# Kernel tuning notes

Measured on AMD Instinct MI355X. Metric: run time of the kernel, lower is better.

The kernel has to match this reference:

```python
import jax, jax.numpy as jnp
import numpy as np

S, B, D, H, A = 256, 1024, 64, 128, 8  # seq_len, buffer, state_size, hidden, action_size


def _init(key, shape, fan_in):
    bound = 1.0 / np.sqrt(fan_in)
    return jax.random.uniform(key, shape, jnp.float32, -bound, bound)


def setup_inputs() -> dict:
    key = jax.random.key(0)
    ks = jax.random.split(key, 24)
    inp = {"state": jax.random.normal(ks[0], (S, B, D), jnp.float32)}
    # actor / critic MLPs (Linear(D,H) + ReLU + Linear(H,H) + ReLU)
    inp["aw1"] = _init(ks[1], (H, D), D); inp["ab1"] = _init(ks[2], (H,), D)
    inp["aw2"] = _init(ks[3], (H, H), H); inp["ab2"] = _init(ks[4], (H,), H)
    inp["cw1"] = _init(ks[5], (H, D), D); inp["cb1"] = _init(ks[6], (H,), D)
    inp["cw2"] = _init(ks[7], (H, H), H); inp["cb2"] = _init(ks[8], (H,), H)
    # LSTMs (PyTorch layout: W_ih [4H,H], W_hh [4H,H], gate order i,f,g,o)
    inp["a_wih"] = _init(ks[9], (4 * H, H), H); inp["a_whh"] = _init(ks[10], (4 * H, H), H)
    inp["a_bih"] = _init(ks[11], (4 * H,), H); inp["a_bhh"] = _init(ks[12], (4 * H,), H)
    inp["c_wih"] = _init(ks[13], (4 * H, H), H); inp["c_whh"] = _init(ks[14], (4 * H, H), H)
    inp["c_bih"] = _init(ks[15], (4 * H,), H); inp["c_bhh"] = _init(ks[16], (4 * H,), H)
    # heads
    inp["mw"] = _init(ks[17], (A, H), H); inp["mb"] = _init(ks[18], (A,), H)
    inp["lw"] = _init(ks[19], (A, H), H); inp["lb"] = _init(ks[20], (A,), H)
    inp["vw"] = _init(ks[21], (1, H), H); inp["vb"] = _init(ks[22], (1,), H)
    return inp


def _mlp(x, w1, b1, w2, b2):
    h = jax.nn.relu(jnp.einsum('sbd,hd->sbh', x, w1) + b1)
    return jax.nn.relu(jnp.einsum('sbh,gh->sbg', h, w2) + b2)


def _lstm_zero_state(x, w_ih, b_ih, b_hh):
    # Each timestep runs with fresh zero (h, c): the recurrent term vanishes,
    # so the whole sequence is one batched GEMM + gating (W_hh unused).
    gates = jnp.einsum('sbh,gh->sbg', x, w_ih) + b_ih + b_hh  # [S,B,4H]
    i, f, g, o = jnp.split(gates, 4, axis=-1)
    c = jax.nn.sigmoid(i) * jnp.tanh(g)  # f * c_prev = 0
    return jax.nn.sigmoid(o) * jnp.tanh(c)


def reference(state, aw1, ab1, aw2, ab2, cw1, cb1, cw2, cb2,
              a_wih, a_whh, a_bih, a_bhh, c_wih, c_whh, c_bih, c_bhh,
              mw, mb, lw, lb, vw, vb):
    actor_h = _lstm_zero_state(_mlp(state, aw1, ab1, aw2, ab2), a_wih, a_bih, a_bhh)
    critic_h = _lstm_zero_state(_mlp(state, cw1, cb1, cw2, cb2), c_wih, c_bih, c_bhh)
    mean = jnp.einsum('sbh,ah->sba', actor_h, mw) + mb
    std = jnp.exp(jnp.einsum('sbh,ah->sba', actor_h, lw) + lb)
    value = jnp.einsum('sbh,vh->sbv', critic_h, vw) + vb
    return (mean, std, value)
```

## Files before the change

kernel.cpp:

```cpp
#include <hip/hip_runtime.h>


#define NROWS (256 * 1024)
#define HID 128
#define ACTD 8

#define W1_OFF 0
#define W2_OFF 16384
#define WI_OFF 49152
#define WG_OFF 81920
#define WO_OFF 114688
#define PSTR 147456
#define HEAD_OFF (2 * PSTR)
#define GB_OFF (HEAD_OFF + 8192)

#define NEG_L (-1.4426950408889634f)
#define TWO_L (2.8853900817779268f)

typedef __attribute__((ext_vector_type(8))) short s16x8;
typedef __attribute__((ext_vector_type(4))) float fx4;
typedef __attribute__((ext_vector_type(2))) unsigned int u32x2;
typedef __attribute__((ext_vector_type(4))) unsigned int u32x4;

__device__ __forceinline__ unsigned int cvtpk(float lo, float hi) {
  unsigned int r;
  asm("v_cvt_pk_bf16_f32 %0, %1, %2" : "=v"(r) : "v"(lo), "v"(hi));
  return r;
}
__device__ __forceinline__ float ex2(float x) {
  return __builtin_amdgcn_exp2f(x);
}
__device__ __forceinline__ float frcp(float x) {
  return __builtin_amdgcn_rcpf(x);
}

__device__ __forceinline__ s16x8 frag_ld(const unsigned short* base, int row,
                                         int kbyte, int rowsh) {
  int byte = (row << rowsh) + (kbyte ^ ((row & 7) << 4));
  return *(const s16x8*)((const char*)base + byte);
}

struct wpair {
  s16x8 w0, w1;
};
template <int KC>
__device__ __forceinline__ wpair wload(const char* __restrict__ wimg, int wv,
                                       int kc, int woff) {
  wpair p;
  p.w0 = *(const s16x8*)(wimg + (((wv * 2 + 0) * KC + kc) << 10) + woff);
  p.w1 = *(const s16x8*)(wimg + (((wv * 2 + 1) * KC + kc) << 10) + woff);
  return p;
}

template <int ASH>
__device__ __forceinline__ void gemm_kc(const wpair& p,
                                        const unsigned short* at, int kbyte,
                                        int l15, fx4 acc[4][2]) {
#pragma unroll
  for (int jt = 0; jt < 4; ++jt) {
    s16x8 a = frag_ld(at, jt * 16 + l15, kbyte, ASH);
    acc[jt][0] = __builtin_amdgcn_mfma_f32_16x16x32_bf16(p.w0, a, acc[jt][0], 0, 0, 0);
    acc[jt][1] = __builtin_amdgcn_mfma_f32_16x16x32_bf16(p.w1, a, acc[jt][1], 0, 0, 0);
  }
}

__device__ __forceinline__ void zacc(fx4 acc[4][2]) {
#pragma unroll
  for (int j = 0; j < 4; ++j)
#pragma unroll
    for (int i = 0; i < 2; ++i) acc[j][i] = fx4{0.f, 0.f, 0.f, 0.f};
}
__device__ __forceinline__ void bacc(fx4 acc[4][2], const float* __restrict__ b,
                                     int fb, int g4) {
#pragma unroll
  for (int it = 0; it < 2; ++it) {
    fx4 bv = *(const fx4*)(b + fb + it * 16 + g4);
#pragma unroll
    for (int jt = 0; jt < 4; ++jt) acc[jt][it] = bv;
  }
}

__device__ __forceinline__ void epi_relu(fx4 acc[4][2], unsigned short* obuf,
                                         int fb, int lane) {
  const int g4 = (lane >> 4) << 2;
  const int l15 = lane & 15;
  char* ob = (char*)obuf;
#pragma unroll
  for (int it = 0; it < 2; ++it) {
    int n0 = fb + it * 16 + g4;
#pragma unroll
    for (int jt = 0; jt < 4; ++jt) {
      fx4 v = acc[jt][it];
#pragma unroll
      for (int r = 0; r < 4; ++r) v[r] = fmaxf(v[r], 0.0f);
      u32x2 u;
      u[0] = cvtpk(v[0], v[1]);
      u[1] = cvtpk(v[2], v[3]);
      int m = jt * 16 + l15;
      *(u32x2*)(ob + (m << 8) + ((n0 * 2) ^ ((m & 7) << 4))) = u;
    }
  }
}

__global__ void prep_weights(const float* __restrict__ aw1,
                             const float* __restrict__ aw2,
                             const float* __restrict__ awih,
                             const float* __restrict__ cw1,
                             const float* __restrict__ cw2,
                             const float* __restrict__ cwih,
                             const float* __restrict__ mw,
                             const float* __restrict__ lw,
                             const float* __restrict__ vw,
                             const float* __restrict__ abih,
                             const float* __restrict__ abhh,
                             const float* __restrict__ cbih,
                             const float* __restrict__ cbhh,
                             char* __restrict__ ws) {
  int y = blockIdx.y;
  int idx = blockIdx.x * 256 + threadIdx.x;
  if (y >= 12) {
    if (idx < 384) {
      float* dst = (float*)(ws + GB_OFF + (size_t)(y - 12) * 1536);
      const float* b0 = (y == 12) ? abih : cbih;
      const float* b1 = (y == 12) ? abhh : cbhh;
      int sect = idx >> 7, f = idx & 127;
      int srow = (sect == 0) ? f : (sect == 1) ? 256 + f : 384 + f;
      float scale = (sect == 1) ? TWO_L : NEG_L;
      dst[idx] = scale * (b0[srow] + b1[srow]);
    }
    return;
  }
  if (y >= 10) {
    if (idx >= 256) return;
    int row = idx >> 4, c16 = idx & 15, kc = c16 >> 2, ks = c16 & 3;
    fx4 v0 = {0.f, 0.f, 0.f, 0.f}, v1 = v0;
    if (y == 10) {
      const float* src = (row < 8) ? (mw + (size_t)row * HID + c16 * 8)
                                   : (lw + (size_t)(row - 8) * HID + c16 * 8);
      v0 = ((const fx4*)src)[0];
      v1 = ((const fx4*)src)[1];
    } else if (row == 0) {
      const float* src = vw + c16 * 8;
      v0 = ((const fx4*)src)[0];
      v1 = ((const fx4*)src)[1];
    }
    u32x4 u;
    u[0] = cvtpk(v0[0], v0[1]);
    u[1] = cvtpk(v0[2], v0[3]);
    u[2] = cvtpk(v1[0], v1[1]);
    u[3] = cvtpk(v1[2], v1[3]);
    int dst = ((kc * 4 + ks) * 16 + row) * 16;
    *(u32x4*)(ws + HEAD_OFF + (size_t)(y - 10) * 4096 + dst) = u;
    return;
  }
  const float* src;
  int nch, ksh, KC, off;
  switch (y) {
    case 0:  src = aw1;              nch = 1024; ksh = 3; KC = 2; off = W1_OFF;        break;
    case 1:  src = aw2;              nch = 2048; ksh = 4; KC = 4; off = W2_OFF;        break;
    case 2:  src = awih;             nch = 2048; ksh = 4; KC = 4; off = WI_OFF;        break;
    case 3:  src = awih + 256 * HID; nch = 2048; ksh = 4; KC = 4; off = WG_OFF;        break;
    case 4:  src = awih + 384 * HID; nch = 2048; ksh = 4; KC = 4; off = WO_OFF;        break;
    case 5:  src = cw1;              nch = 1024; ksh = 3; KC = 2; off = PSTR + W1_OFF; break;
    case 6:  src = cw2;              nch = 2048; ksh = 4; KC = 4; off = PSTR + W2_OFF; break;
    case 7:  src = cwih;             nch = 2048; ksh = 4; KC = 4; off = PSTR + WI_OFF; break;
    case 8:  src = cwih + 256 * HID; nch = 2048; ksh = 4; KC = 4; off = PSTR + WG_OFF; break;
    default: src = cwih + 384 * HID; nch = 2048; ksh = 4; KC = 4; off = PSTR + WO_OFF; break;
  }
  if (idx >= nch) return;
  int row = idx >> ksh;
  int c16 = idx & ((1 << ksh) - 1);
  int b2 = row >> 4, r = row & 15, kc = c16 >> 2, ks = c16 & 3;
  const fx4* gp = (const fx4*)(src + (size_t)idx * 8);
  fx4 v0 = gp[0], v1 = gp[1];
  u32x4 u;
  u[0] = cvtpk(v0[0], v0[1]);
  u[1] = cvtpk(v0[2], v0[3]);
  u[2] = cvtpk(v1[0], v1[1]);
  u[3] = cvtpk(v1[2], v1[3]);
  int dst = (((b2 * KC + kc) * 4 + ks) * 16 + r) * 16;
  *(u32x4*)(ws + off + dst) = u;
}

__global__ __launch_bounds__(256, 3) void fused_ac(
    const float* __restrict__ state, const float* __restrict__ ab1,
    const float* __restrict__ ab2, const float* __restrict__ cb1,
    const float* __restrict__ cb2, const float* __restrict__ mb,
    const float* __restrict__ lb, const float* __restrict__ vb,
    const char* __restrict__ ws, float* __restrict__ outp) {
  __shared__ __align__(16) unsigned short abuf[8192];
  __shared__ __align__(16) unsigned short hbuf[8192];

  const int tid = threadIdx.x;
  const int lane = tid & 63;
  const int wv = tid >> 6;
  const int l15 = lane & 15;
  const int g4 = (lane >> 4) << 2;
  const int kb0 = (lane >> 4) << 4;
  const int woff = ((lane >> 4) << 8) + (l15 << 4);
  const int fb = wv << 5;
  const int path = blockIdx.x >> 12;
  const int rbase = (blockIdx.x & 4095) << 6;

  const char* wsp = ws + (size_t)path * PSTR;
  const float* b1 = path ? cb1 : ab1;
  const float* b2 = path ? cb2 : ab2;
  const float* gb = (const float*)(ws + GB_OFF + (size_t)path * 1536);
  const char* himg = ws + HEAD_OFF + (size_t)path * 4096;

  float* meanp = outp;
  float* stdp = outp + (size_t)NROWS * ACTD;
  float* valp = outp + (size_t)NROWS * ACTD * 2;

  wpair w1a = wload<2>(wsp + W1_OFF, wv, 0, woff);
  wpair w1b = wload<2>(wsp + W1_OFF, wv, 1, woff);

  {
    const float* xg = state + (size_t)rbase * 64;
    char* ab = (char*)abuf;
#pragma unroll
    for (int i = 0; i < 2; ++i) {
      int idx = tid + i * 256;
      int r = idx >> 3, c = idx & 7;
      const fx4* gp = (const fx4*)(xg + idx * 8);
      fx4 v0 = gp[0], v1 = gp[1];
      u32x4 u;
      u[0] = cvtpk(v0[0], v0[1]);
      u[1] = cvtpk(v0[2], v0[3]);
      u[2] = cvtpk(v1[0], v1[1]);
      u[3] = cvtpk(v1[2], v1[3]);
      *(u32x4*)(ab + r * 128 + ((c << 4) ^ ((r & 7) << 4))) = u;
    }
  }
  __syncthreads();

  fx4 acc[4][2];
  bacc(acc, b1, fb, g4);
  gemm_kc<7>(w1a, abuf, 0 + kb0, l15, acc);
  gemm_kc<7>(w1b, abuf, 64 + kb0, l15, acc);
  wpair w2a = wload<4>(wsp + W2_OFF, wv, 0, woff);
  wpair w2b = wload<4>(wsp + W2_OFF, wv, 1, woff);
  epi_relu(acc, hbuf, fb, lane);
  __syncthreads();

  bacc(acc, b2, fb, g4);
  gemm_kc<8>(w2a, hbuf, 0 + kb0, l15, acc);
  gemm_kc<8>(w2b, hbuf, 64 + kb0, l15, acc);
  {
    wpair p = wload<4>(wsp + W2_OFF, wv, 2, woff);
    gemm_kc<8>(p, hbuf, 128 + kb0, l15, acc);
  }
  {
    wpair p = wload<4>(wsp + W2_OFF, wv, 3, woff);
    gemm_kc<8>(p, hbuf, 192 + kb0, l15, acc);
  }
  wpair wia = wload<4>(wsp + WI_OFF, wv, 0, woff);
  wpair wib = wload<4>(wsp + WI_OFF, wv, 1, woff);
  epi_relu(acc, abuf, fb, lane);
  __syncthreads();

  fx4 carry[4][2];
  zacc(acc);
  gemm_kc<8>(wia, abuf, 0 + kb0, l15, acc);
  gemm_kc<8>(wib, abuf, 64 + kb0, l15, acc);
  {
    wpair p = wload<4>(wsp + WI_OFF, wv, 2, woff);
    gemm_kc<8>(p, abuf, 128 + kb0, l15, acc);
  }
  {
    wpair p = wload<4>(wsp + WI_OFF, wv, 3, woff);
    gemm_kc<8>(p, abuf, 192 + kb0, l15, acc);
  }
#pragma unroll
  for (int it = 0; it < 2; ++it) {
    fx4 pv = *(const fx4*)(gb + fb + it * 16 + g4);
#pragma unroll
    for (int jt = 0; jt < 4; ++jt)
#pragma unroll
      for (int r = 0; r < 4; ++r)
        carry[jt][it][r] = ex2(fmaf(acc[jt][it][r], NEG_L, pv[r]));
  }

  zacc(acc);
#pragma unroll
  for (int kc = 0; kc < 4; ++kc) {
    wpair p = wload<4>(wsp + WG_OFF, wv, kc, woff);
    gemm_kc<8>(p, abuf, kc * 64 + kb0, l15, acc);
  }
#pragma unroll
  for (int it = 0; it < 2; ++it) {
    fx4 pv = *(const fx4*)(gb + 128 + fb + it * 16 + g4);
#pragma unroll
    for (int jt = 0; jt < 4; ++jt)
#pragma unroll
      for (int r = 0; r < 4; ++r) {
        float Eg = ex2(fmaf(acc[jt][it][r], TWO_L, pv[r]));
        float c = (Eg - 1.0f) * frcp((Eg + 1.0f) * (carry[jt][it][r] + 1.0f));
        carry[jt][it][r] = ex2(c * TWO_L);
      }
  }

  zacc(acc);
#pragma unroll
  for (int kc = 0; kc < 4; ++kc) {
    wpair p = wload<4>(wsp + WO_OFF, wv, kc, woff);
    gemm_kc<8>(p, abuf, kc * 64 + kb0, l15, acc);
  }
  s16x8 hw0 = *(const s16x8*)(himg + (0 << 10) + woff);
  s16x8 hw1 = *(const s16x8*)(himg + (1 << 10) + woff);
  s16x8 hw2 = *(const s16x8*)(himg + (2 << 10) + woff);
  s16x8 hw3 = *(const s16x8*)(himg + (3 << 10) + woff);
  {
    char* ob = (char*)hbuf;
#pragma unroll
    for (int it = 0; it < 2; ++it) {
      fx4 pv = *(const fx4*)(gb + 256 + fb + it * 16 + g4);
      int n0 = fb + it * 16 + g4;
#pragma unroll
      for (int jt = 0; jt < 4; ++jt) {
        fx4 h;
#pragma unroll
        for (int r = 0; r < 4; ++r) {
          float Eo = ex2(fmaf(acc[jt][it][r], NEG_L, pv[r]));
          float Ec = carry[jt][it][r];
          h[r] = (Ec - 1.0f) * frcp((Ec + 1.0f) * (Eo + 1.0f));
        }
        u32x2 u;
        u[0] = cvtpk(h[0], h[1]);
        u[1] = cvtpk(h[2], h[3]);
        int m = jt * 16 + l15;
        *(u32x2*)(ob + (m << 8) + ((n0 * 2) ^ ((m & 7) << 4))) = u;
      }
    }
  }
  __syncthreads();

  fx4 ha = fx4{0.f, 0.f, 0.f, 0.f};
  ha = __builtin_amdgcn_mfma_f32_16x16x32_bf16(
      hw0, frag_ld(hbuf, (wv << 4) + l15, 0 + kb0, 8), ha, 0, 0, 0);
  ha = __builtin_amdgcn_mfma_f32_16x16x32_bf16(
      hw1, frag_ld(hbuf, (wv << 4) + l15, 64 + kb0, 8), ha, 0, 0, 0);
  ha = __builtin_amdgcn_mfma_f32_16x16x32_bf16(
      hw2, frag_ld(hbuf, (wv << 4) + l15, 128 + kb0, 8), ha, 0, 0, 0);
  ha = __builtin_amdgcn_mfma_f32_16x16x32_bf16(
      hw3, frag_ld(hbuf, (wv << 4) + l15, 192 + kb0, 8), ha, 0, 0, 0);

  int m = rbase + (wv << 4) + l15;
  if (path == 0) {
    if (g4 < 8) {
      fx4 v = ha + *(const fx4*)(mb + g4);
      *(fx4*)(meanp + (size_t)m * ACTD + g4) = v;
    } else {
      fx4 v;
#pragma unroll
      for (int r = 0; r < 4; ++r) v[r] = __expf(ha[r] + lb[g4 - 8 + r]);
      *(fx4*)(stdp + (size_t)m * ACTD + (g4 - 8)) = v;
    }
  } else if (g4 == 0) {
    valp[m] = ha[0] + vb[0];
  }
}

extern "C" void kernel_launch(void* const* d_in, const int* in_sizes, int n_in,
                              void* d_out, int out_size, void* d_ws,
                              size_t ws_size, hipStream_t stream) {
  (void)in_sizes; (void)n_in; (void)ws_size; (void)out_size;
  const float* state = (const float*)d_in[0];
  const float* aw1 = (const float*)d_in[1];
  const float* ab1 = (const float*)d_in[2];
  const float* aw2 = (const float*)d_in[3];
  const float* ab2 = (const float*)d_in[4];
  const float* cw1 = (const float*)d_in[5];
  const float* cb1 = (const float*)d_in[6];
  const float* cw2 = (const float*)d_in[7];
  const float* cb2 = (const float*)d_in[8];
  const float* awih = (const float*)d_in[9];
  const float* abih = (const float*)d_in[11];
  const float* abhh = (const float*)d_in[12];
  const float* cwih = (const float*)d_in[13];
  const float* cbih = (const float*)d_in[15];
  const float* cbhh = (const float*)d_in[16];
  const float* mw = (const float*)d_in[17];
  const float* mb = (const float*)d_in[18];
  const float* lw = (const float*)d_in[19];
  const float* lb = (const float*)d_in[20];
  const float* vw = (const float*)d_in[21];
  const float* vb = (const float*)d_in[22];
  char* ws = (char*)d_ws;

  prep_weights<<<dim3(8, 14), 256, 0, stream>>>(
      aw1, aw2, awih, cw1, cw2, cwih, mw, lw, vw, abih, abhh, cbih, cbhh, ws);
  fused_ac<<<8192, 256, 0, stream>>>(state, ab1, ab2, cb1, cb2, mb, lb, vb, ws,
                                     (float*)d_out);
}
```

Measured before the change: 120.1 us.

## Split work across 8 waves per block, one 16-column tile each

Doubles the block to 512 threads so each of the 8 waves computes a single 16-wide feature slice instead of two. This halves per-wave accumulator and weight registers and raises the number of resident waves. The state load now uses one element per thread, and only the first four waves run the head GEMM. In exchange, each wave reloads the shared activation fragments for half as much MFMA work, so LDS traffic per MFMA doubles, and the head phase leaves half the waves idle.

```diff
diff --git a/kernel.cpp b/kernel.cpp
--- a/kernel.cpp
+++ b/kernel.cpp
@@ -40,65 +40,50 @@
   return *(const s16x8*)((const char*)base + byte);
 }
 
-struct wpair {
-  s16x8 w0, w1;
-};
 template <int KC>
-__device__ __forceinline__ wpair wload(const char* __restrict__ wimg, int wv,
-                                       int kc, int woff) {
-  wpair p;
-  p.w0 = *(const s16x8*)(wimg + (((wv * 2 + 0) * KC + kc) << 10) + woff);
-  p.w1 = *(const s16x8*)(wimg + (((wv * 2 + 1) * KC + kc) << 10) + woff);
-  return p;
+__device__ __forceinline__ s16x8 wload1(const char* __restrict__ wimg, int wv,
+                                        int kc, int woff) {
+  return *(const s16x8*)(wimg + ((wv * KC + kc) << 10) + woff);
 }
 
 template <int ASH>
-__device__ __forceinline__ void gemm_kc(const wpair& p,
+__device__ __forceinline__ void gemm_kc(const s16x8 w,
                                         const unsigned short* at, int kbyte,
-                                        int l15, fx4 acc[4][2]) {
+                                        int l15, fx4 acc[4]) {
 #pragma unroll
   for (int jt = 0; jt < 4; ++jt) {
     s16x8 a = frag_ld(at, jt * 16 + l15, kbyte, ASH);
-    acc[jt][0] = __builtin_amdgcn_mfma_f32_16x16x32_bf16(p.w0, a, acc[jt][0], 0, 0, 0);
-    acc[jt][1] = __builtin_amdgcn_mfma_f32_16x16x32_bf16(p.w1, a, acc[jt][1], 0, 0, 0);
-  }
-}
-
-__device__ __forceinline__ void zacc(fx4 acc[4][2]) {
-#pragma unroll
-  for (int j = 0; j < 4; ++j)
-#pragma unroll
-    for (int i = 0; i < 2; ++i) acc[j][i] = fx4{0.f, 0.f, 0.f, 0.f};
-}
-__device__ __forceinline__ void bacc(fx4 acc[4][2], const float* __restrict__ b,
+    acc[jt] = __builtin_amdgcn_mfma_f32_16x16x32_bf16(w, a, acc[jt], 0, 0, 0);
+  }
+}
+
+__device__ __forceinline__ void zacc(fx4 acc[4]) {
+#pragma unroll
+  for (int j = 0; j < 4; ++j) acc[j] = fx4{0.f, 0.f, 0.f, 0.f};
+}
+__device__ __forceinline__ void bacc(fx4 acc[4], const float* __restrict__ b,
                                      int fb, int g4) {
-#pragma unroll
-  for (int it = 0; it < 2; ++it) {
-    fx4 bv = *(const fx4*)(b + fb + it * 16 + g4);
-#pragma unroll
-    for (int jt = 0; jt < 4; ++jt) acc[jt][it] = bv;
-  }
-}
-
-__device__ __forceinline__ void epi_relu(fx4 acc[4][2], unsigned short* obuf,
+  fx4 bv = *(const fx4*)(b + fb + g4);
+#pragma unroll
+  for (int jt = 0; jt < 4; ++jt) acc[jt] = bv;
+}
+
+__device__ __forceinline__ void epi_relu(fx4 acc[4], unsigned short* obuf,
                                          int fb, int lane) {
   const int g4 = (lane >> 4) << 2;
   const int l15 = lane & 15;
+  const int n0 = fb + g4;
   char* ob = (char*)obuf;
 #pragma unroll
-  for (int it = 0; it < 2; ++it) {
-    int n0 = fb + it * 16 + g4;
-#pragma unroll
-    for (int jt = 0; jt < 4; ++jt) {
-      fx4 v = acc[jt][it];
-#pragma unroll
-      for (int r = 0; r < 4; ++r) v[r] = fmaxf(v[r], 0.0f);
-      u32x2 u;
-      u[0] = cvtpk(v[0], v[1]);
-      u[1] = cvtpk(v[2], v[3]);
-      int m = jt * 16 + l15;
-      *(u32x2*)(ob + (m << 8) + ((n0 * 2) ^ ((m & 7) << 4))) = u;
-    }
+  for (int jt = 0; jt < 4; ++jt) {
+    fx4 v = acc[jt];
+#pragma unroll
+    for (int r = 0; r < 4; ++r) v[r] = fmaxf(v[r], 0.0f);
+    u32x2 u;
+    u[0] = cvtpk(v[0], v[1]);
+    u[1] = cvtpk(v[2], v[3]);
+    int m = jt * 16 + l15;
+    *(u32x2*)(ob + (m << 8) + ((n0 * 2) ^ ((m & 7) << 4))) = u;
   }
 }
 
@@ -182,7 +167,7 @@
   *(u32x4*)(ws + off + dst) = u;
 }
 
-__global__ __launch_bounds__(256, 3) void fused_ac(
+__global__ __launch_bounds__(512, 4) void fused_ac(
     const float* __restrict__ state, const float* __restrict__ ab1,
     const float* __restrict__ ab2, const float* __restrict__ cb1,
     const float* __restrict__ cb2, const float* __restrict__ mb,
@@ -198,7 +183,7 @@
   const int g4 = (lane >> 4) << 2;
   const int kb0 = (lane >> 4) << 4;
   const int woff = ((lane >> 4) << 8) + (l15 << 4);
-  const int fb = wv << 5;
+  const int fb = wv << 4;
   const int path = blockIdx.x >> 12;
   const int rbase = (blockIdx.x & 4095) << 6;
 
@@ -212,152 +197,134 @@
   float* stdp = outp + (size_t)NROWS * ACTD;
   float* valp = outp + (size_t)NROWS * ACTD * 2;
 
-  wpair w1a = wload<2>(wsp + W1_OFF, wv, 0, woff);
-  wpair w1b = wload<2>(wsp + W1_OFF, wv, 1, woff);
+  s16x8 w1a = wload1<2>(wsp + W1_OFF, wv, 0, woff);
+  s16x8 w1b = wload1<2>(wsp + W1_OFF, wv, 1, woff);
 
   {
     const float* xg = state + (size_t)rbase * 64;
     char* ab = (char*)abuf;
-#pragma unroll
-    for (int i = 0; i < 2; ++i) {
-      int idx = tid + i * 256;
-      int r = idx >> 3, c = idx & 7;
-      const fx4* gp = (const fx4*)(xg + idx * 8);
-      fx4 v0 = gp[0], v1 = gp[1];
-      u32x4 u;
-      u[0] = cvtpk(v0[0], v0[1]);
-      u[1] = cvtpk(v0[2], v0[3]);
-      u[2] = cvtpk(v1[0], v1[1]);
-      u[3] = cvtpk(v1[2], v1[3]);
-      *(u32x4*)(ab + r * 128 + ((c << 4) ^ ((r & 7) << 4))) = u;
-    }
+    int r = tid >> 3, c = tid & 7;
+    const fx4* gp = (const fx4*)(xg + tid * 8);
+    fx4 v0 = gp[0], v1 = gp[1];
+    u32x4 u;
+    u[0] = cvtpk(v0[0], v0[1]);
+    u[1] = cvtpk(v0[2], v0[3]);
+    u[2] = cvtpk(v1[0], v1[1]);
+    u[3] = cvtpk(v1[2], v1[3]);
+    *(u32x4*)(ab + r * 128 + ((c << 4) ^ ((r & 7) << 4))) = u;
   }
   __syncthreads();
 
-  fx4 acc[4][2];
+  fx4 acc[4];
   bacc(acc, b1, fb, g4);
   gemm_kc<7>(w1a, abuf, 0 + kb0, l15, acc);
   gemm_kc<7>(w1b, abuf, 64 + kb0, l15, acc);
-  wpair w2a = wload<4>(wsp + W2_OFF, wv, 0, woff);
-  wpair w2b = wload<4>(wsp + W2_OFF, wv, 1, woff);
+  s16x8 w2a = wload1<4>(wsp + W2_OFF, wv, 0, woff);
+  s16x8 w2b = wload1<4>(wsp + W2_OFF, wv, 1, woff);
   epi_relu(acc, hbuf, fb, lane);
   __syncthreads();
 
   bacc(acc, b2, fb, g4);
   gemm_kc<8>(w2a, hbuf, 0 + kb0, l15, acc);
   gemm_kc<8>(w2b, hbuf, 64 + kb0, l15, acc);
-  {
-    wpair p = wload<4>(wsp + W2_OFF, wv, 2, woff);
-    gemm_kc<8>(p, hbuf, 128 + kb0, l15, acc);
-  }
-  {
-    wpair p = wload<4>(wsp + W2_OFF, wv, 3, woff);
-    gemm_kc<8>(p, hbuf, 192 + kb0, l15, acc);
-  }
-  wpair wia = wload<4>(wsp + WI_OFF, wv, 0, woff);
-  wpair wib = wload<4>(wsp + WI_OFF, wv, 1, woff);
+  gemm_kc<8>(wload1<4>(wsp + W2_OFF, wv, 2, woff), hbuf, 128 + kb0, l15, acc);
+  gemm_kc<8>(wload1<4>(wsp + W2_OFF, wv, 3, woff), hbuf, 192 + kb0, l15, acc);
+  s16x8 wia = wload1<4>(wsp + WI_OFF, wv, 0, woff);
+  s16x8 wib = wload1<4>(wsp + WI_OFF, wv, 1, woff);
   epi_relu(acc, abuf, fb, lane);
   __syncthreads();
 
-  fx4 carry[4][2];
+  fx4 carry[4];
   zacc(acc);
   gemm_kc<8>(wia, abuf, 0 + kb0, l15, acc);
   gemm_kc<8>(wib, abuf, 64 + kb0, l15, acc);
+  gemm_kc<8>(wload1<4>(wsp + WI_OFF, wv, 2, woff), abuf, 128 + kb0, l15, acc);
+  gemm_kc<8>(wload1<4>(wsp + WI_OFF, wv, 3, woff), abuf, 192 + kb0, l15, acc);
   {
-    wpair p = wload<4>(wsp + WI_OFF, wv, 2, woff);
-    gemm_kc<8>(p, abuf, 128 + kb0, l15, acc);
-  }
+    fx4 pv = *(const fx4*)(gb + fb + g4);
+#pragma unroll
+    for (int jt = 0; jt < 4; ++jt)
+#pragma unroll
+      for (int r = 0; r < 4; ++r)
+        carry[jt][r] = ex2(fmaf(acc[jt][r], NEG_L, pv[r]));
+  }
+
+  zacc(acc);
+#pragma unroll
+  for (int kc = 0; kc < 4; ++kc)
+    gemm_kc<8>(wload1<4>(wsp + WG_OFF, wv, kc, woff), abuf, kc * 64 + kb0,
+               l15, acc);
   {
-    wpair p = wload<4>(wsp + WI_OFF, wv, 3, woff);
-    gemm_kc<8>(p, abuf, 192 + kb0, l15, acc);
-  }
-#pragma unroll
-  for (int it = 0; it < 2; ++it) {
-    fx4 pv = *(const fx4*)(gb + fb + it * 16 + g4);
+    fx4 pv = *(const fx4*)(gb + 128 + fb + g4);
 #pragma unroll
     for (int jt = 0; jt < 4; ++jt)
 #pragma unroll
-      for (int r = 0; r < 4; ++r)
-        carry[jt][it][r] = ex2(fmaf(acc[jt][it][r], NEG_L, pv[r]));
+      for (int r = 0; r < 4; ++r) {
+        float Eg = ex2(fmaf(acc[jt][r], TWO_L, pv[r]));
+        float c = (Eg - 1.0f) * frcp((Eg + 1.0f) * (carry[jt][r] + 1.0f));
+        carry[jt][r] = ex2(c * TWO_L);
+      }
   }
 
   zacc(acc);
 #pragma unroll
-  for (int kc = 0; kc < 4; ++kc) {
-    wpair p = wload<4>(wsp + WG_OFF, wv, kc, woff);
-    gemm_kc<8>(p, abuf, kc * 64 + kb0, l15, acc);
-  }
-#pragma unroll
-  for (int it = 0; it < 2; ++it) {
-    fx4 pv = *(const fx4*)(gb + 128 + fb + it * 16 + g4);
-#pragma unroll
-    for (int jt = 0; jt < 4; ++jt)
-#pragma unroll
-      for (int r = 0; r < 4; ++r) {
-        float Eg = ex2(fmaf(acc[jt][it][r], TWO_L, pv[r]));
-        float c = (Eg - 1.0f) * frcp((Eg + 1.0f) * (carry[jt][it][r] + 1.0f));
-        carry[jt][it][r] = ex2(c * TWO_L);
-      }
-  }
-
-  zacc(acc);
-#pragma unroll
-  for (int kc = 0; kc < 4; ++kc) {
-    wpair p = wload<4>(wsp + WO_OFF, wv, kc, woff);
-    gemm_kc<8>(p, abuf, kc * 64 + kb0, l15, acc);
-  }
-  s16x8 hw0 = *(const s16x8*)(himg + (0 << 10) + woff);
-  s16x8 hw1 = *(const s16x8*)(himg + (1 << 10) + woff);
-  s16x8 hw2 = *(const s16x8*)(himg + (2 << 10) + woff);
-  s16x8 hw3 = *(const s16x8*)(himg + (3 << 10) + woff);
+  for (int kc = 0; kc < 4; ++kc)
+    gemm_kc<8>(wload1<4>(wsp + WO_OFF, wv, kc, woff), abuf, kc * 64 + kb0,
+               l15, acc);
+  s16x8 hw0, hw1, hw2, hw3;
+  if (wv < 4) {
+    hw0 = *(const s16x8*)(himg + (0 << 10) + woff);
+    hw1 = *(const s16x8*)(himg + (1 << 10) + woff);
+    hw2 = *(const s16x8*)(himg + (2 << 10) + woff);
+    hw3 = *(const s16x8*)(himg + (3 << 10) + woff);
+  }
   {
     char* ob = (char*)hbuf;
-#pragma unroll
-    for (int it = 0; it < 2; ++it) {
-      fx4 pv = *(const fx4*)(gb + 256 + fb + it * 16 + g4);
-      int n0 = fb + it * 16 + g4;
-#pragma unroll
-      for (int jt = 0; jt < 4; ++jt) {
-        fx4 h;
-#pragma unroll
-        for (int r = 0; r < 4; ++r) {
-          float Eo = ex2(fmaf(acc[jt][it][r], NEG_L, pv[r]));
-          float Ec = carry[jt][it][r];
-          h[r] = (Ec - 1.0f) * frcp((Ec + 1.0f) * (Eo + 1.0f));
-        }
-        u32x2 u;
-        u[0] = cvtpk(h[0], h[1]);
-        u[1] = cvtpk(h[2], h[3]);
-        int m = jt * 16 + l15;
-        *(u32x2*)(ob + (m << 8) + ((n0 * 2) ^ ((m & 7) << 4))) = u;
+    fx4 pv = *(const fx4*)(gb + 256 + fb + g4);
+    const int n0 = fb + g4;
+#pragma unroll
+    for (int jt = 0; jt < 4; ++jt) {
+      fx4 h;
+#pragma unroll
+      for (int r = 0; r < 4; ++r) {
+        float Eo = ex2(fmaf(acc[jt][r], NEG_L, pv[r]));
+        float Ec = carry[jt][r];
+        h[r] = (Ec - 1.0f) * frcp((Ec + 1.0f) * (Eo + 1.0f));
       }
+      u32x2 u;
+      u[0] = cvtpk(h[0], h[1]);
+      u[1] = cvtpk(h[2], h[3]);
+      int m = jt * 16 + l15;
+      *(u32x2*)(ob + (m << 8) + ((n0 * 2) ^ ((m & 7) << 4))) = u;
     }
   }
   __syncthreads();
 
-  fx4 ha = fx4{0.f, 0.f, 0.f, 0.f};
-  ha = __builtin_amdgcn_mfma_f32_16x16x32_bf16(
-      hw0, frag_ld(hbuf, (wv << 4) + l15, 0 + kb0, 8), ha, 0, 0, 0);
-  ha = __builtin_amdgcn_mfma_f32_16x16x32_bf16(
-      hw1, frag_ld(hbuf, (wv << 4) + l15, 64 + kb0, 8), ha, 0, 0, 0);
-  ha = __builtin_amdgcn_mfma_f32_16x16x32_bf16(
-      hw2, frag_ld(hbuf, (wv << 4) + l15, 128 + kb0, 8), ha, 0, 0, 0);
-  ha = __builtin_amdgcn_mfma_f32_16x16x32_bf16(
-      hw3, frag_ld(hbuf, (wv << 4) + l15, 192 + kb0, 8), ha, 0, 0, 0);
-
-  int m = rbase + (wv << 4) + l15;
-  if (path == 0) {
-    if (g4 < 8) {
-      fx4 v = ha + *(const fx4*)(mb + g4);
-      *(fx4*)(meanp + (size_t)m * ACTD + g4) = v;
-    } else {
-      fx4 v;
-#pragma unroll
-      for (int r = 0; r < 4; ++r) v[r] = __expf(ha[r] + lb[g4 - 8 + r]);
-      *(fx4*)(stdp + (size_t)m * ACTD + (g4 - 8)) = v;
+  if (wv < 4) {
+    fx4 ha = fx4{0.f, 0.f, 0.f, 0.f};
+    ha = __builtin_amdgcn_mfma_f32_16x16x32_bf16(
+        hw0, frag_ld(hbuf, (wv << 4) + l15, 0 + kb0, 8), ha, 0, 0, 0);
+    ha = __builtin_amdgcn_mfma_f32_16x16x32_bf16(
+        hw1, frag_ld(hbuf, (wv << 4) + l15, 64 + kb0, 8), ha, 0, 0, 0);
+    ha = __builtin_amdgcn_mfma_f32_16x16x32_bf16(
+        hw2, frag_ld(hbuf, (wv << 4) + l15, 128 + kb0, 8), ha, 0, 0, 0);
+    ha = __builtin_amdgcn_mfma_f32_16x16x32_bf16(
+        hw3, frag_ld(hbuf, (wv << 4) + l15, 192 + kb0, 8), ha, 0, 0, 0);
+
+    int m = rbase + (wv << 4) + l15;
+    if (path == 0) {
+      if (g4 < 8) {
+        fx4 v = ha + *(const fx4*)(mb + g4);
+        *(fx4*)(meanp + (size_t)m * ACTD + g4) = v;
+      } else {
+        fx4 v;
+#pragma unroll
+        for (int r = 0; r < 4; ++r) v[r] = __expf(ha[r] + lb[g4 - 8 + r]);
+        *(fx4*)(stdp + (size_t)m * ACTD + (g4 - 8)) = v;
+      }
+    } else if (g4 == 0) {
+      valp[m] = ha[0] + vb[0];
     }
-  } else if (g4 == 0) {
-    valp[m] = ha[0] + vb[0];
   }
 }
 
@@ -390,6 +357,6 @@
 
   prep_weights<<<dim3(8, 14), 256, 0, stream>>>(
       aw1, aw2, awih, cw1, cw2, cwih, mw, lw, vw, abih, abhh, cbih, cbhh, ws);
-  fused_ac<<<8192, 256, 0, stream>>>(state, ab1, ab2, cb1, cb2, mb, lb, vb, ws,
+  fused_ac<<<8192, 512, 0, stream>>>(state, ab1, ab2, cb1, cb2, mb, lb, vb, ws,
                                      (float*)d_out);
 }
```

New measurement: 128.9 us. 1.07x slower.

## Fuse the three LSTM gate GEMMs into one K loop sharing A fragments

Applied to the files above, without the earlier changes.

The i, g and o gate GEMMs are merged into a single K loop. Each activation fragment loaded from LDS now feeds all three gates' MFMAs, instead of being reloaded in three separate passes. The gating math moves into a single epilogue. This cuts LDS fragment reads by a factor of three and gives the scheduler more independent MFMAs, but triples live accumulator registers (24 fx4 accumulators plus weight pairs), which risks lower occupancy or spills.

```diff
diff --git a/kernel.cpp b/kernel.cpp
--- a/kernel.cpp
+++ b/kernel.cpp
@@ -254,75 +254,56 @@
     wpair p = wload<4>(wsp + W2_OFF, wv, 3, woff);
     gemm_kc<8>(p, hbuf, 192 + kb0, l15, acc);
   }
-  wpair wia = wload<4>(wsp + WI_OFF, wv, 0, woff);
-  wpair wib = wload<4>(wsp + WI_OFF, wv, 1, woff);
+  wpair pi0 = wload<4>(wsp + WI_OFF, wv, 0, woff);
+  wpair pg0 = wload<4>(wsp + WG_OFF, wv, 0, woff);
+  wpair po0 = wload<4>(wsp + WO_OFF, wv, 0, woff);
   epi_relu(acc, abuf, fb, lane);
   __syncthreads();
 
-  fx4 carry[4][2];
-  zacc(acc);
-  gemm_kc<8>(wia, abuf, 0 + kb0, l15, acc);
-  gemm_kc<8>(wib, abuf, 64 + kb0, l15, acc);
-  {
-    wpair p = wload<4>(wsp + WI_OFF, wv, 2, woff);
-    gemm_kc<8>(p, abuf, 128 + kb0, l15, acc);
-  }
-  {
-    wpair p = wload<4>(wsp + WI_OFF, wv, 3, woff);
-    gemm_kc<8>(p, abuf, 192 + kb0, l15, acc);
-  }
-#pragma unroll
-  for (int it = 0; it < 2; ++it) {
-    fx4 pv = *(const fx4*)(gb + fb + it * 16 + g4);
-#pragma unroll
-    for (int jt = 0; jt < 4; ++jt)
-#pragma unroll
-      for (int r = 0; r < 4; ++r)
-        carry[jt][it][r] = ex2(fmaf(acc[jt][it][r], NEG_L, pv[r]));
-  }
-
-  zacc(acc);
+  fx4 ai[4][2], ag[4][2], ao[4][2];
+  zacc(ai);
+  zacc(ag);
+  zacc(ao);
 #pragma unroll
   for (int kc = 0; kc < 4; ++kc) {
-    wpair p = wload<4>(wsp + WG_OFF, wv, kc, woff);
-    gemm_kc<8>(p, abuf, kc * 64 + kb0, l15, acc);
-  }
-#pragma unroll
-  for (int it = 0; it < 2; ++it) {
-    fx4 pv = *(const fx4*)(gb + 128 + fb + it * 16 + g4);
-#pragma unroll
-    for (int jt = 0; jt < 4; ++jt)
-#pragma unroll
-      for (int r = 0; r < 4; ++r) {
-        float Eg = ex2(fmaf(acc[jt][it][r], TWO_L, pv[r]));
-        float c = (Eg - 1.0f) * frcp((Eg + 1.0f) * (carry[jt][it][r] + 1.0f));
-        carry[jt][it][r] = ex2(c * TWO_L);
-      }
-  }
-
-  zacc(acc);
-#pragma unroll
-  for (int kc = 0; kc < 4; ++kc) {
-    wpair p = wload<4>(wsp + WO_OFF, wv, kc, woff);
-    gemm_kc<8>(p, abuf, kc * 64 + kb0, l15, acc);
+    wpair pi = (kc == 0) ? pi0 : wload<4>(wsp + WI_OFF, wv, kc, woff);
+    wpair pg = (kc == 0) ? pg0 : wload<4>(wsp + WG_OFF, wv, kc, woff);
+    wpair po = (kc == 0) ? po0 : wload<4>(wsp + WO_OFF, wv, kc, woff);
+    int kbyte = kc * 64 + kb0;
+#pragma unroll
+    for (int jt = 0; jt < 4; ++jt) {
+      s16x8 a = frag_ld(abuf, jt * 16 + l15, kbyte, 8);
+      ai[jt][0] = __builtin_amdgcn_mfma_f32_16x16x32_bf16(pi.w0, a, ai[jt][0], 0, 0, 0);
+      ai[jt][1] = __builtin_amdgcn_mfma_f32_16x16x32_bf16(pi.w1, a, ai[jt][1], 0, 0, 0);
+      ag[jt][0] = __builtin_amdgcn_mfma_f32_16x16x32_bf16(pg.w0, a, ag[jt][0], 0, 0, 0);
+      ag[jt][1] = __builtin_amdgcn_mfma_f32_16x16x32_bf16(pg.w1, a, ag[jt][1], 0, 0, 0);
+      ao[jt][0] = __builtin_amdgcn_mfma_f32_16x16x32_bf16(po.w0, a, ao[jt][0], 0, 0, 0);
+      ao[jt][1] = __builtin_amdgcn_mfma_f32_16x16x32_bf16(po.w1, a, ao[jt][1], 0, 0, 0);
+    }
   }
   s16x8 hw0 = *(const s16x8*)(himg + (0 << 10) + woff);
   s16x8 hw1 = *(const s16x8*)(himg + (1 << 10) + woff);
   s16x8 hw2 = *(const s16x8*)(himg + (2 << 10) + woff);
   s16x8 hw3 = *(const s16x8*)(himg + (3 << 10) + woff);
+
   {
     char* ob = (char*)hbuf;
 #pragma unroll
     for (int it = 0; it < 2; ++it) {
-      fx4 pv = *(const fx4*)(gb + 256 + fb + it * 16 + g4);
+      fx4 pvi = *(const fx4*)(gb + fb + it * 16 + g4);
+      fx4 pvg = *(const fx4*)(gb + 128 + fb + it * 16 + g4);
+      fx4 pvo = *(const fx4*)(gb + 256 + fb + it * 16 + g4);
       int n0 = fb + it * 16 + g4;
 #pragma unroll
       for (int jt = 0; jt < 4; ++jt) {
         fx4 h;
 #pragma unroll
         for (int r = 0; r < 4; ++r) {
-          float Eo = ex2(fmaf(acc[jt][it][r], NEG_L, pv[r]));
-          float Ec = carry[jt][it][r];
+          float Ei = ex2(fmaf(ai[jt][it][r], NEG_L, pvi[r]));
+          float Eg = ex2(fmaf(ag[jt][it][r], TWO_L, pvg[r]));
+          float Eo = ex2(fmaf(ao[jt][it][r], NEG_L, pvo[r]));
+          float c = (Eg - 1.0f) * frcp((Eg + 1.0f) * (Ei + 1.0f));
+          float Ec = ex2(c * TWO_L);
           h[r] = (Ec - 1.0f) * frcp((Ec + 1.0f) * (Eo + 1.0f));
         }
         u32x2 u;
```

After: 118.6 us. No clear change (-1.2%).
